# Performance work log

Hardware: AMD Instinct MI355X
Metric: run time of the kernel (lower is better)

The kernel has to match this reference:

```python
import jax, jax.numpy as jnp
import numpy as np

TWO_PI = 2.0 * np.pi
SIGMA = 25.0  # marginal_prob_std sigma


def marginal_prob_std(t):
    # std(t) = sqrt((sigma^{2t} - 1) / (2 ln sigma)) for VE-SDE
    return jnp.sqrt((SIGMA ** (2.0 * t) - 1.0) / (2.0 * np.log(SIGMA)))


def edge_conv(x, src, dst, W1, b1, W2, b2, num_nodes):
    # PyG EdgeConv: msg = mlp(cat([x_i, x_j - x_i])), x_i = x[dst], x_j = x[src];
    # scatter-max over dst. First linear split so concat is never materialized:
    # cat([x_i, x_j - x_i]) @ W1 = x_i @ (Wa - Wb) + x_j @ Wb
    d = x.shape[-1]
    Wa, Wb = W1[:d], W1[d:]
    h_center = x @ (Wa - Wb)        # [N, H]
    h_nbr = x @ Wb                  # [N, H]
    e = jax.nn.relu(h_center[dst] + h_nbr[src] + b1)  # [E, H]
    e = e @ W2 + b2                 # [E, out]
    return jax.ops.segment_max(e, dst, num_segments=num_nodes)


def setup_inputs() -> dict:
    N, E, B, H, EM = 50000, 500000, 1024, 128, 64
    CLS, SD, GD, WD = 10, 4, 2, 2
    key = jax.random.key(0)
    ks = jax.random.split(key, 32)

    def lin(k, fi, fo):
        return jax.random.normal(k, (fi, fo), jnp.float32) / np.sqrt(fi)

    inp = {
        "t": jax.random.uniform(ks[0], (N, 1), jnp.float32, 1e-3, 1.0),
        "obj_x": jax.random.normal(ks[1], (N, SD), jnp.float32),
        "obj_geo": jax.random.normal(ks[2], (N, GD), jnp.float32),
        "wall": jax.random.normal(ks[3], (B, WD), jnp.float32),
        "category": jax.random.randint(ks[4], (N,), 0, CLS),
        "batch_idx": jnp.sort(jax.random.randint(ks[5], (N,), 0, B)),
        "src": jax.random.randint(ks[6], (E,), 0, N),
        "dst": jnp.tile(jnp.arange(N), E // N),  # every node receives edges
        "embed_W": jax.random.normal(ks[7], (CLS, EM), jnp.float32),
        "gfp_W": jax.random.normal(ks[8], (EM // 2,), jnp.float32) * 30.0,
        "sW": lin(ks[9], EM, EM), "sb": jnp.zeros((EM,), jnp.float32),
        "w1": lin(ks[10], WD, EM), "wb1": jnp.zeros((EM,), jnp.float32),
        "w2": lin(ks[11], EM, EM), "wb2": jnp.zeros((EM,), jnp.float32),
        "i1": lin(ks[12], SD + GD, H), "ib1": jnp.zeros((H,), jnp.float32),
        "i2": lin(ks[13], H, H), "ib2": jnp.zeros((H,), jnp.float32),
        "m1W1": lin(ks[14], 2 * (H + 3 * EM), H), "m1b1": jnp.zeros((H,), jnp.float32),
        "m1W2": lin(ks[15], H, H), "m1b2": jnp.zeros((H,), jnp.float32),
        "m2W1": lin(ks[16], 2 * (H + 3 * EM), H), "m2b1": jnp.zeros((H,), jnp.float32),
        "m2W2": lin(ks[17], H, SD), "m2b2": jnp.zeros((SD,), jnp.float32),
    }
    return inp


def reference(t, obj_x, obj_geo, wall, category, batch_idx, src, dst,
              embed_W, gfp_W, sW, sb, w1, wb1, w2, wb2,
              i1, ib1, i2, ib2, m1W1, m1b1, m1W2, m1b2,
              m2W1, m2b1, m2W2, m2b2):
    N = obj_x.shape[0]
    # conditioning features
    class_feat = jax.nn.relu(embed_W[category])                       # [N, EM]
    tv = t[:, 0]                                                      # [N]
    x_proj = tv[:, None] * gfp_W[None, :] * TWO_PI                    # [N, EM/2]
    gfp = jnp.concatenate([jnp.sin(x_proj), jnp.cos(x_proj)], axis=-1)
    sigma_feat = jax.nn.relu(gfp @ sW + sb)                           # [N, EM]
    wall_h = jax.nn.relu(jax.nn.relu(wall @ w1 + wb1) @ w2 + wb2)     # [B, EM]
    wall_feat = wall_h[batch_idx]                                     # [N, EM]
    cond = jnp.concatenate([class_feat, sigma_feat, wall_feat], axis=-1)

    # init encoder
    xin = jnp.concatenate([obj_x, obj_geo], axis=-1)                  # [N, 6]
    init = jax.nn.relu(jax.nn.relu(xin @ i1 + ib1) @ i2 + ib2)        # [N, H]

    # main backbone: two EdgeConvs with conditioning concat
    x = jnp.concatenate([init, cond], axis=-1)                        # [N, H+3EM]
    x = jax.nn.relu(edge_conv(x, src, dst, m1W1, m1b1, m1W2, m1b2, N))
    x = jnp.concatenate([x, cond], axis=-1)                           # [N, H+3EM]
    x = edge_conv(x, src, dst, m2W1, m2b1, m2W2, m2b2, N)             # [N, 4]

    return x / (marginal_prob_std(t) + 1e-7)
```

## Files before the change

kernel.cpp:

```cpp
#include <hip/hip_runtime.h>
#include <hip/hip_bf16.h>
#include <math.h>

#define NTHREADS 256
#define TWO_PI_F 6.28318530717958647692f
#define LOG_SIGMA 3.2188758248682006f

typedef unsigned short u16;
typedef unsigned int u32;
typedef short bf16x8 __attribute__((ext_vector_type(8)));
typedef float f32x4 __attribute__((ext_vector_type(4)));

#define MFMA(a, b, c) __builtin_amdgcn_mfma_f32_16x16x32_bf16((a), (b), (c), 0, 0, 0)

__device__ __forceinline__ u16 f2b(float f) {
  __hip_bfloat16 h = __float2bfloat16(f);
  return __builtin_bit_cast(u16, h);
}
__device__ __forceinline__ u32 pk2(float lo, float hi) {
  return (u32)f2b(lo) | ((u32)f2b(hi) << 16);
}
__device__ __forceinline__ float blo(u32 u) { return __uint_as_float(u << 16); }
__device__ __forceinline__ float bhi(u32 u) { return __uint_as_float(u & 0xffff0000u); }

__global__ __launch_bounds__(256) void prep_wall_kernel(
    const float* __restrict__ m1W2, const float* __restrict__ m1W1,
    const float* __restrict__ m2W1, const float* __restrict__ sW,
    const float* __restrict__ i1, const float* __restrict__ i2,
    const float* __restrict__ wall, const float* __restrict__ w1,
    const float* __restrict__ wb1, const float* __restrict__ w2,
    const float* __restrict__ wb2,
    u16* __restrict__ m1W2t, u16* __restrict__ Wc1t, u16* __restrict__ Wc2t,
    u16* __restrict__ sWt, u16* __restrict__ i1t, u16* __restrict__ i2t,
    float* __restrict__ wall_h, int B) {
  if (blockIdx.x >= 800) {
    __shared__ float h1[4][64];
    int g = threadIdx.x >> 6, f = threadIdx.x & 63;
    int b = (blockIdx.x - 800) * 4 + g;
    if (b < B) {
      float v = wall[b * 2 + 0] * w1[f] + wall[b * 2 + 1] * w1[64 + f] + wb1[f];
      h1[g][f] = fmaxf(v, 0.f);
    }
    __syncthreads();
    if (b < B) {
      float acc = wb2[f];
      for (int k = 0; k < 64; ++k) acc = fmaf(h1[g][k], w2[k * 64 + f], acc);
      wall_h[b * 64 + f] = fmaxf(acc, 0.f);
    }
    return;
  }
  int idx = blockIdx.x * 256 + threadIdx.x;
  if (idx < 16384) {
    int n = idx >> 7, k = idx & 127;
    m1W2t[idx] = f2b(m1W2[k * 128 + n]);
  } else if (idx < 98304) {
    int j = idx - 16384;
    int n = j / 320, k = j - n * 320;
    float v = (n < 128) ? (m1W1[k * 128 + n] - m1W1[(320 + k) * 128 + n])
                        : m1W1[(320 + k) * 128 + (n - 128)];
    Wc1t[j] = f2b(v);
  } else if (idx < 180224) {
    int j = idx - 98304;
    int n = j / 320, k = j - n * 320;
    float v = (n < 128) ? (m2W1[k * 128 + n] - m2W1[(320 + k) * 128 + n])
                        : m2W1[(320 + k) * 128 + (n - 128)];
    Wc2t[j] = f2b(v);
  } else if (idx < 184320) {
    int j = idx - 180224;
    int n = j >> 6, k = j & 63;
    sWt[j] = f2b(sW[k * 64 + n]);
  } else if (idx < 188416) {
    int j = idx - 184320;
    int n = j >> 5, k = j & 31;
    i1t[j] = (k < 6) ? f2b(i1[k * 128 + n]) : (u16)0;
  } else if (idx < 204800) {
    int j = idx - 188416;
    int n = j >> 7, k = j & 127;
    i2t[j] = f2b(i2[k * 128 + n]);
  }
}

__global__ __launch_bounds__(256) void node_kernel(
    const float* __restrict__ t, const float* __restrict__ obj_x,
    const float* __restrict__ obj_geo,
    const int* __restrict__ category, const int* __restrict__ batch_idx,
    const float* __restrict__ embed_W, const float* __restrict__ gfp_W,
    const u16* __restrict__ sWt, const float* __restrict__ sb,
    const u16* __restrict__ i1t, const float* __restrict__ ib1,
    const u16* __restrict__ i2t, const float* __restrict__ ib2,
    const u16* __restrict__ Wc1t, const float* __restrict__ m1b1,
    const float* __restrict__ wall_h,
    float* __restrict__ hc1, u16* __restrict__ hn1,
    u16* __restrict__ cond_bf, int N) {
  __shared__ u16 xb[64 * 328];
  __shared__ u16 ab[64 * 136];
  __shared__ float t_s[64];
  __shared__ int cat_s[64];
  __shared__ int bid_s[64];

  const int tid = threadIdx.x;
  const int base = blockIdx.x * 64;
  const int wave = tid >> 6, lane = tid & 63;
  const int ln16 = lane & 15, q8 = lane >> 4;

  bf16x8 bs0 = *(const bf16x8*)(sWt + (size_t)((wave * 16 + ln16) * 64) + q8 * 8);
  bf16x8 bs1 = *(const bf16x8*)(sWt + (size_t)((wave * 16 + ln16) * 64) + 32 + q8 * 8);
  bf16x8 bh[2];
#pragma unroll
  for (int nt = 0; nt < 2; ++nt)
    bh[nt] = *(const bf16x8*)(i1t + (size_t)((wave * 32 + nt * 16 + ln16) * 32) + q8 * 8);

  if (tid < 64) {
    int node = min(base + tid, N - 1);
    t_s[tid] = t[node];
    cat_s[tid] = category[node];
    bid_s[tid] = batch_idx[node];
  }
  __syncthreads();

  for (int idx = tid; idx < 64 * 32; idx += NTHREADS) {
    int row = idx >> 5, k = idx & 31;
    float xp = t_s[row] * gfp_W[k] * TWO_PI_F;
    float s, c;
    sincosf(xp, &s, &c);
    ab[row * 136 + k] = f2b(s);
    ab[row * 136 + 32 + k] = f2b(c);
  }
  for (int idx = tid; idx < 64 * 64; idx += NTHREADS) {
    int row = idx >> 6, f = idx & 63;
    xb[row * 328 + 128 + f] = f2b(fmaxf(embed_W[cat_s[row] * 64 + f], 0.f));
    xb[row * 328 + 256 + f] = f2b(wall_h[bid_s[row] * 64 + f]);
  }
  __syncthreads();

  f32x4 cs[4];
#pragma unroll
  for (int mt = 0; mt < 4; ++mt) cs[mt] = (f32x4)0.f;
#pragma unroll
  for (int mt = 0; mt < 4; ++mt) {
    bf16x8 a0 = *(const bf16x8*)&ab[(mt * 16 + ln16) * 136 + q8 * 8];
    cs[mt] = MFMA(a0, bs0, cs[mt]);
  }
#pragma unroll
  for (int mt = 0; mt < 4; ++mt) {
    bf16x8 a1 = *(const bf16x8*)&ab[(mt * 16 + ln16) * 136 + 32 + q8 * 8];
    cs[mt] = MFMA(a1, bs1, cs[mt]);
  }
  __syncthreads();

  {
    int col = wave * 16 + ln16;
    float bias = sb[col];
#pragma unroll
    for (int mt = 0; mt < 4; ++mt)
#pragma unroll
      for (int r = 0; r < 4; ++r)
        xb[(mt * 16 + q8 * 4 + r) * 328 + 192 + col] = f2b(fmaxf(cs[mt][r] + bias, 0.f));
  }
  for (int idx = tid; idx < 64 * 32; idx += NTHREADS) {
    int row = idx >> 5, k = idx & 31;
    int node = min(base + row, N - 1);
    float v = (k < 4) ? obj_x[node * 4 + k] : ((k < 6) ? obj_geo[node * 2 + (k - 4)] : 0.f);
    ab[row * 136 + k] = f2b(v);
  }
  __syncthreads();

  for (int idx = tid; idx < 64 * 24; idx += NTHREADS) {
    int row = idx / 24, q = idx - row * 24;
    int node = base + row;
    if (node < N)
      *(uint4*)&cond_bf[(size_t)node * 192 + q * 8] = *(uint4*)&xb[row * 328 + 128 + q * 8];
  }

  f32x4 ch[2][4];
#pragma unroll
  for (int nt = 0; nt < 2; ++nt)
#pragma unroll
    for (int mt = 0; mt < 4; ++mt) ch[nt][mt] = (f32x4)0.f;
#pragma unroll
  for (int mt = 0; mt < 4; ++mt) {
    bf16x8 a = *(const bf16x8*)&ab[(mt * 16 + ln16) * 136 + q8 * 8];
#pragma unroll
    for (int nt = 0; nt < 2; ++nt) ch[nt][mt] = MFMA(a, bh[nt], ch[nt][mt]);
  }
  bf16x8 bcur2[2], bnext2[2];
#pragma unroll
  for (int nt = 0; nt < 2; ++nt)
    bcur2[nt] = *(const bf16x8*)(i2t + (size_t)((wave * 32 + nt * 16 + ln16) * 128) + q8 * 8);
  __syncthreads();
#pragma unroll
  for (int nt = 0; nt < 2; ++nt) {
    int col = wave * 32 + nt * 16 + ln16;
    float bias = ib1[col];
#pragma unroll
    for (int mt = 0; mt < 4; ++mt)
#pragma unroll
      for (int r = 0; r < 4; ++r)
        ab[(mt * 16 + q8 * 4 + r) * 136 + col] = f2b(fmaxf(ch[nt][mt][r] + bias, 0.f));
  }
  __syncthreads();

  f32x4 ci[2][4];
#pragma unroll
  for (int nt = 0; nt < 2; ++nt)
#pragma unroll
    for (int mt = 0; mt < 4; ++mt) ci[nt][mt] = (f32x4)0.f;
  for (int kt = 0; kt < 4; ++kt) {
    if (kt < 3) {
#pragma unroll
      for (int nt = 0; nt < 2; ++nt)
        bnext2[nt] = *(const bf16x8*)(i2t + (size_t)((wave * 32 + nt * 16 + ln16) * 128) +
                                      (kt + 1) * 32 + q8 * 8);
    }
#pragma unroll
    for (int mt = 0; mt < 4; ++mt) {
      bf16x8 a = *(const bf16x8*)&ab[(mt * 16 + ln16) * 136 + kt * 32 + q8 * 8];
#pragma unroll
      for (int nt = 0; nt < 2; ++nt) ci[nt][mt] = MFMA(a, bcur2[nt], ci[nt][mt]);
    }
#pragma unroll
    for (int nt = 0; nt < 2; ++nt) bcur2[nt] = bnext2[nt];
  }
#pragma unroll
  for (int nt = 0; nt < 2; ++nt) {
    int col = wave * 32 + nt * 16 + ln16;
    float bias = ib2[col];
#pragma unroll
    for (int mt = 0; mt < 4; ++mt)
#pragma unroll
      for (int r = 0; r < 4; ++r)
        xb[(mt * 16 + q8 * 4 + r) * 328 + col] = f2b(fmaxf(ci[nt][mt][r] + bias, 0.f));
  }
  __syncthreads();

  f32x4 c2[4][4];
#pragma unroll
  for (int nt = 0; nt < 4; ++nt)
#pragma unroll
    for (int mt = 0; mt < 4; ++mt) c2[nt][mt] = (f32x4)0.f;
  bf16x8 bcur[4], bnext[4];
#pragma unroll
  for (int nt = 0; nt < 4; ++nt)
    bcur[nt] = *(const bf16x8*)(Wc1t + (size_t)((wave * 64 + nt * 16 + ln16) * 320) + q8 * 8);
  for (int kt = 0; kt < 10; ++kt) {
    if (kt < 9) {
#pragma unroll
      for (int nt = 0; nt < 4; ++nt)
        bnext[nt] = *(const bf16x8*)(Wc1t + (size_t)((wave * 64 + nt * 16 + ln16) * 320) +
                                     (kt + 1) * 32 + q8 * 8);
    }
#pragma unroll
    for (int mt = 0; mt < 4; ++mt) {
      bf16x8 a = *(const bf16x8*)&xb[(mt * 16 + ln16) * 328 + kt * 32 + q8 * 8];
#pragma unroll
      for (int nt = 0; nt < 4; ++nt) c2[nt][mt] = MFMA(a, bcur[nt], c2[nt][mt]);
    }
#pragma unroll
    for (int nt = 0; nt < 4; ++nt) bcur[nt] = bnext[nt];
  }
#pragma unroll
  for (int nt = 0; nt < 4; ++nt) {
    int col = wave * 64 + nt * 16 + ln16;
#pragma unroll
    for (int mt = 0; mt < 4; ++mt)
#pragma unroll
      for (int r = 0; r < 4; ++r) {
        int node = base + mt * 16 + q8 * 4 + r;
        if (node < N) {
          if (col < 128)
            hc1[(size_t)node * 128 + col] = c2[nt][mt][r] + m1b1[col];
          else
            hn1[(size_t)node * 128 + (col - 128)] = f2b(c2[nt][mt][r]);
        }
      }
  }
}

__device__ __forceinline__ void pack_edge(u16* __restrict__ dst, const float* __restrict__ hcr,
                                          uint4 g0, uint4 g1, int ln, int kq) {
  float a[16];
  a[0] = blo(g0.x); a[1] = bhi(g0.x); a[2] = blo(g0.y); a[3] = bhi(g0.y);
  a[4] = blo(g0.z); a[5] = bhi(g0.z); a[6] = blo(g0.w); a[7] = bhi(g0.w);
  a[8] = blo(g1.x); a[9] = bhi(g1.x); a[10] = blo(g1.y); a[11] = bhi(g1.y);
  a[12] = blo(g1.z); a[13] = bhi(g1.z); a[14] = blo(g1.w); a[15] = bhi(g1.w);
#pragma unroll
  for (int i = 0; i < 16; ++i) a[i] = fmaxf(hcr[i] + a[i], 0.f);
  uint4 o0, o1;
  o0.x = pk2(a[0], a[1]); o0.y = pk2(a[2], a[3]); o0.z = pk2(a[4], a[5]); o0.w = pk2(a[6], a[7]);
  o1.x = pk2(a[8], a[9]); o1.y = pk2(a[10], a[11]); o1.z = pk2(a[12], a[13]); o1.w = pk2(a[14], a[15]);
  *(uint4*)&dst[ln * 136 + kq * 16] = o0;
  *(uint4*)&dst[ln * 136 + kq * 16 + 8] = o1;
}

__global__ __launch_bounds__(256) void edge1_kernel(
    const float* __restrict__ hc1, const u16* __restrict__ hn1,
    const u16* __restrict__ cond_bf, const int* __restrict__ src,
    const u16* __restrict__ m1W2t, const float* __restrict__ m1b2,
    const u16* __restrict__ Wc2t, const float* __restrict__ m2b1,
    float* __restrict__ hc2, u16* __restrict__ hn2, int N) {
  __shared__ u16 a_lds[2][32 * 136];
  __shared__ u16 x2_lds[32 * 328];
  __shared__ int sid[320];

  const int tid = threadIdx.x;
  const int base = blockIdx.x * 32;
  const int wave = tid >> 6, lane = tid & 63;
  const int ln16 = lane & 15, q8 = lane >> 4;

  for (int idx = tid; idx < 320; idx += NTHREADS) {
    int e = idx >> 5, n = idx & 31;
    int node = min(base + n, N - 1);
    sid[idx] = src[node + e * N];
  }
  for (int idx = tid; idx < 768; idx += NTHREADS) {
    int n = idx / 24, q = idx - n * 24;
    int node = min(base + n, N - 1);
    *(uint4*)&x2_lds[n * 328 + 128 + q * 8] = *(const uint4*)&cond_bf[(size_t)node * 192 + q * 8];
  }
  const int ln = tid >> 3, kq = tid & 7;
  const int lnode = min(base + ln, N - 1);
  float hcr[16];
#pragma unroll
  for (int q = 0; q < 4; ++q) {
    float4 v = *(const float4*)&hc1[(size_t)lnode * 128 + kq * 16 + q * 4];
    hcr[q * 4 + 0] = v.x; hcr[q * 4 + 1] = v.y; hcr[q * 4 + 2] = v.z; hcr[q * 4 + 3] = v.w;
  }
  bf16x8 bfrag[2][4];
#pragma unroll
  for (int nt = 0; nt < 2; ++nt)
#pragma unroll
    for (int kt = 0; kt < 4; ++kt)
      bfrag[nt][kt] = *(const bf16x8*)(m1W2t + (size_t)((2 * wave + nt) * 16 + ln16) * 128 +
                                       kt * 32 + q8 * 8);

  f32x4 ymax[2][2];
#pragma unroll
  for (int mt = 0; mt < 2; ++mt)
#pragma unroll
    for (int nt = 0; nt < 2; ++nt)
#pragma unroll
      for (int r = 0; r < 4; ++r) ymax[mt][nt][r] = -3.0e38f;

  __syncthreads();

  {
    int s0 = sid[ln];
    uint4 g0 = *(const uint4*)&hn1[(size_t)s0 * 128 + kq * 16];
    uint4 g1 = *(const uint4*)&hn1[(size_t)s0 * 128 + kq * 16 + 8];
    pack_edge(&a_lds[0][0], hcr, g0, g1, ln, kq);
  }
  uint4 gA0, gA1, gB0, gB1;
  {
    int s1 = sid[32 + ln];
    gA0 = *(const uint4*)&hn1[(size_t)s1 * 128 + kq * 16];
    gA1 = *(const uint4*)&hn1[(size_t)s1 * 128 + kq * 16 + 8];
    int s2 = sid[64 + ln];
    gB0 = *(const uint4*)&hn1[(size_t)s2 * 128 + kq * 16];
    gB1 = *(const uint4*)&hn1[(size_t)s2 * 128 + kq * 16 + 8];
  }
  asm volatile("s_waitcnt lgkmcnt(0)" ::: "memory");
  __builtin_amdgcn_s_barrier();

#pragma unroll 2
  for (int e = 0; e < 10; ++e) {
    const u16* abuf = &a_lds[e & 1][0];
    f32x4 c[2][2];
#pragma unroll
    for (int mt = 0; mt < 2; ++mt)
#pragma unroll
      for (int nt = 0; nt < 2; ++nt) c[mt][nt] = (f32x4)0.f;
#pragma unroll
    for (int kt = 0; kt < 4; ++kt) {
      bf16x8 a0 = *(const bf16x8*)&abuf[ln16 * 136 + kt * 32 + q8 * 8];
      bf16x8 a1 = *(const bf16x8*)&abuf[(16 + ln16) * 136 + kt * 32 + q8 * 8];
#pragma unroll
      for (int nt = 0; nt < 2; ++nt) {
        c[0][nt] = MFMA(a0, bfrag[nt][kt], c[0][nt]);
        c[1][nt] = MFMA(a1, bfrag[nt][kt], c[1][nt]);
      }
    }
#pragma unroll
    for (int mt = 0; mt < 2; ++mt)
#pragma unroll
      for (int nt = 0; nt < 2; ++nt)
#pragma unroll
        for (int r = 0; r < 4; ++r) ymax[mt][nt][r] = fmaxf(ymax[mt][nt][r], c[mt][nt][r]);

    if (e < 9) {
      if ((e & 1) == 0) {
        pack_edge(&a_lds[1][0], hcr, gA0, gA1, ln, kq);
        if (e + 3 < 10) {
          int s = sid[(e + 3) * 32 + ln];
          gA0 = *(const uint4*)&hn1[(size_t)s * 128 + kq * 16];
          gA1 = *(const uint4*)&hn1[(size_t)s * 128 + kq * 16 + 8];
        }
      } else {
        pack_edge(&a_lds[0][0], hcr, gB0, gB1, ln, kq);
        if (e + 3 < 10) {
          int s = sid[(e + 3) * 32 + ln];
          gB0 = *(const uint4*)&hn1[(size_t)s * 128 + kq * 16];
          gB1 = *(const uint4*)&hn1[(size_t)s * 128 + kq * 16 + 8];
        }
      }
      asm volatile("s_waitcnt lgkmcnt(0)" ::: "memory");
      __builtin_amdgcn_s_barrier();
    }
  }

#pragma unroll
  for (int mt = 0; mt < 2; ++mt)
#pragma unroll
    for (int nt = 0; nt < 2; ++nt) {
      int col = (2 * wave + nt) * 16 + ln16;
      float bias = m1b2[col];
#pragma unroll
      for (int r = 0; r < 4; ++r) {
        int row = mt * 16 + q8 * 4 + r;
        x2_lds[row * 328 + col] = f2b(fmaxf(ymax[mt][nt][r] + bias, 0.f));
      }
    }
  __syncthreads();

  f32x4 c2[2][4];
#pragma unroll
  for (int mt = 0; mt < 2; ++mt)
#pragma unroll
    for (int nt = 0; nt < 4; ++nt) c2[mt][nt] = (f32x4)0.f;
  bf16x8 bcur[4], bnext[4];
#pragma unroll
  for (int nt = 0; nt < 4; ++nt)
    bcur[nt] = *(const bf16x8*)(Wc2t + (size_t)((wave * 4 + nt) * 16 + ln16) * 320 + q8 * 8);
  for (int kt = 0; kt < 10; ++kt) {
    if (kt < 9) {
#pragma unroll
      for (int nt = 0; nt < 4; ++nt)
        bnext[nt] = *(const bf16x8*)(Wc2t + (size_t)((wave * 4 + nt) * 16 + ln16) * 320 +
                                     (kt + 1) * 32 + q8 * 8);
    }
    bf16x8 a0 = *(const bf16x8*)&x2_lds[ln16 * 328 + kt * 32 + q8 * 8];
    bf16x8 a1 = *(const bf16x8*)&x2_lds[(16 + ln16) * 328 + kt * 32 + q8 * 8];
#pragma unroll
    for (int nt = 0; nt < 4; ++nt) {
      c2[0][nt] = MFMA(a0, bcur[nt], c2[0][nt]);
      c2[1][nt] = MFMA(a1, bcur[nt], c2[1][nt]);
    }
#pragma unroll
    for (int nt = 0; nt < 4; ++nt) bcur[nt] = bnext[nt];
  }
#pragma unroll
  for (int mt = 0; mt < 2; ++mt)
#pragma unroll
    for (int nt = 0; nt < 4; ++nt) {
      int col = (wave * 4 + nt) * 16 + ln16;
#pragma unroll
      for (int r = 0; r < 4; ++r) {
        int row = mt * 16 + q8 * 4 + r;
        int node = base + row;
        if (node < N) {
          if (wave < 2)
            hc2[(size_t)node * 128 + col] = c2[mt][nt][r] + m2b1[col];
          else
            hn2[(size_t)node * 128 + (col - 128)] = f2b(c2[mt][nt][r]);
        }
      }
    }
}

__global__ __launch_bounds__(256) void edge2_kernel(
    const float* __restrict__ hc2, const u16* __restrict__ hn2,
    const int* __restrict__ src, const float* __restrict__ t,
    const float* __restrict__ m2W2, const float* __restrict__ m2b2,
    float* __restrict__ out, int N) {
  const int tid = threadIdx.x;
  const int base = blockIdx.x * 32;
  const int ln = tid >> 3, kq = tid & 7;
  const int node = min(base + ln, N - 1);

  int s[10];
#pragma unroll
  for (int e = 0; e < 10; ++e) s[e] = src[node + e * N];

  float acc[10][4];
#pragma unroll
  for (int e = 0; e < 10; ++e)
#pragma unroll
    for (int j = 0; j < 4; ++j) acc[e][j] = 0.f;

#pragma unroll
  for (int p = 0; p < 2; ++p) {
    const int d0 = p * 64 + kq * 8;
    float hcr[8];
    {
      float4 v0 = *(const float4*)&hc2[(size_t)node * 128 + d0];
      float4 v1 = *(const float4*)&hc2[(size_t)node * 128 + d0 + 4];
      hcr[0] = v0.x; hcr[1] = v0.y; hcr[2] = v0.z; hcr[3] = v0.w;
      hcr[4] = v1.x; hcr[5] = v1.y; hcr[6] = v1.z; hcr[7] = v1.w;
    }
    float w[8][4];
#pragma unroll
    for (int i = 0; i < 8; ++i) {
      float4 v = *(const float4*)&m2W2[(d0 + i) * 4];
      w[i][0] = v.x; w[i][1] = v.y; w[i][2] = v.z; w[i][3] = v.w;
    }
    uint4 gA = *(const uint4*)&hn2[(size_t)s[0] * 128 + d0];
    uint4 gB = *(const uint4*)&hn2[(size_t)s[1] * 128 + d0];
#pragma unroll
    for (int e = 0; e < 10; ++e) {
      uint4 h = (e & 1) ? gB : gA;
      if (e + 2 < 10) {
        uint4 gn = *(const uint4*)&hn2[(size_t)s[e + 2] * 128 + d0];
        if (e & 1) gB = gn; else gA = gn;
      }
      float a[8];
      a[0] = blo(h.x); a[1] = bhi(h.x); a[2] = blo(h.y); a[3] = bhi(h.y);
      a[4] = blo(h.z); a[5] = bhi(h.z); a[6] = blo(h.w); a[7] = bhi(h.w);
#pragma unroll
      for (int i = 0; i < 8; ++i) {
        float av = fmaxf(hcr[i] + a[i], 0.f);
#pragma unroll
        for (int j = 0; j < 4; ++j) acc[e][j] = fmaf(av, w[i][j], acc[e][j]);
      }
      __builtin_amdgcn_sched_barrier(0);
    }
  }

  float ymax[4] = {-3.0e38f, -3.0e38f, -3.0e38f, -3.0e38f};
#pragma unroll
  for (int e = 0; e < 10; ++e) {
    float t0 = acc[e][0], t1 = acc[e][1], t2 = acc[e][2], t3 = acc[e][3];
#pragma unroll
    for (int mask = 1; mask <= 4; mask <<= 1) {
      t0 += __shfl_xor(t0, mask);
      t1 += __shfl_xor(t1, mask);
      t2 += __shfl_xor(t2, mask);
      t3 += __shfl_xor(t3, mask);
    }
    ymax[0] = fmaxf(ymax[0], t0);
    ymax[1] = fmaxf(ymax[1], t1);
    ymax[2] = fmaxf(ymax[2], t2);
    ymax[3] = fmaxf(ymax[3], t3);
  }
  if (kq < 4 && base + ln < N) {
    float tv = t[node];
    float mps = sqrtf((expf(2.f * tv * LOG_SIGMA) - 1.f) * (1.f / (2.f * LOG_SIGMA)));
    out[(size_t)node * 4 + kq] = (ymax[kq] + m2b2[kq]) / (mps + 1e-7f);
  }
}

extern "C" void kernel_launch(void* const* d_in, const int* in_sizes, int n_in,
                              void* d_out, int out_size, void* d_ws, size_t ws_size,
                              hipStream_t stream) {
  const float* t = (const float*)d_in[0];
  const float* obj_x = (const float*)d_in[1];
  const float* obj_geo = (const float*)d_in[2];
  const float* wall = (const float*)d_in[3];
  const int* category = (const int*)d_in[4];
  const int* batch_idx = (const int*)d_in[5];
  const int* src = (const int*)d_in[6];
  const float* embed_W = (const float*)d_in[8];
  const float* gfp_W = (const float*)d_in[9];
  const float* sW = (const float*)d_in[10];
  const float* sb = (const float*)d_in[11];
  const float* w1 = (const float*)d_in[12];
  const float* wb1 = (const float*)d_in[13];
  const float* w2 = (const float*)d_in[14];
  const float* wb2 = (const float*)d_in[15];
  const float* i1 = (const float*)d_in[16];
  const float* ib1 = (const float*)d_in[17];
  const float* i2 = (const float*)d_in[18];
  const float* ib2 = (const float*)d_in[19];
  const float* m1W1 = (const float*)d_in[20];
  const float* m1b1 = (const float*)d_in[21];
  const float* m1W2 = (const float*)d_in[22];
  const float* m1b2 = (const float*)d_in[23];
  const float* m2W1 = (const float*)d_in[24];
  const float* m2b1 = (const float*)d_in[25];
  const float* m2W2 = (const float*)d_in[26];
  const float* m2b2 = (const float*)d_in[27];
  float* out = (float*)d_out;

  const int N = in_sizes[0];
  const int B = in_sizes[3] / 2;

  char* w = (char*)d_ws;
  float* wall_h = (float*)w; w += (size_t)B * 64 * 4;
  u16* cond_bf = (u16*)w;   w += (size_t)N * 192 * 2;
  float* hc1 = (float*)w;   w += (size_t)N * 128 * 4;
  u16* hn1 = (u16*)w;       w += (size_t)N * 128 * 2;
  float* hc2 = (float*)w;   w += (size_t)N * 128 * 4;
  u16* hn2 = (u16*)w;       w += (size_t)N * 128 * 2;
  u16* m1W2t = (u16*)w;     w += (size_t)128 * 128 * 2;
  u16* Wc1t = (u16*)w;      w += (size_t)256 * 320 * 2;
  u16* Wc2t = (u16*)w;      w += (size_t)256 * 320 * 2;
  u16* sWt = (u16*)w;       w += (size_t)64 * 64 * 2;
  u16* i1t = (u16*)w;       w += (size_t)128 * 32 * 2;
  u16* i2t = (u16*)w;       w += (size_t)128 * 128 * 2;

  int wall_blocks = (B + 3) / 4;
  prep_wall_kernel<<<dim3(800 + wall_blocks), dim3(256), 0, stream>>>(
      m1W2, m1W1, m2W1, sW, i1, i2, wall, w1, wb1, w2, wb2,
      m1W2t, Wc1t, Wc2t, sWt, i1t, i2t, wall_h, B);
  node_kernel<<<dim3((N + 63) / 64), dim3(NTHREADS), 0, stream>>>(
      t, obj_x, obj_geo, category, batch_idx, embed_W, gfp_W, sWt, sb,
      i1t, ib1, i2t, ib2, Wc1t, m1b1, wall_h, hc1, hn1, cond_bf, N);
  edge1_kernel<<<dim3((N + 31) / 32), dim3(NTHREADS), 0, stream>>>(
      hc1, hn1, cond_bf, src, m1W2t, m1b2, Wc2t, m2b1, hc2, hn2, N);
  edge2_kernel<<<dim3((N + 31) / 32), dim3(NTHREADS), 0, stream>>>(
      hc2, hn2, src, t, m2W2, m2b2, out, N);
}
```

Measured before the change: 270.0 us.

## Split edge1 K dimension into halves with per-edge accumulators and finer pipeline

Restructures the edge-message loop in edge1_kernel to gather and pack only half of each neighbor's 128-wide hidden row per step. It runs 20 half-K steps and keeps five per-edge MFMA accumulators, folding them into the running max after each group of five edges. This halves the LDS staging buffer and the per-step gather size, aiming at lower LDS use and a finer-grained gather/MFMA overlap. In exchange it doubles the number of barriers and adds 20 f32x4 accumulator registers, which may reduce occupancy.

```diff
diff --git a/kernel.cpp b/kernel.cpp
--- a/kernel.cpp
+++ b/kernel.cpp
@@ -276,20 +276,16 @@
   }
 }
 
-__device__ __forceinline__ void pack_edge(u16* __restrict__ dst, const float* __restrict__ hcr,
-                                          uint4 g0, uint4 g1, int ln, int kq) {
-  float a[16];
-  a[0] = blo(g0.x); a[1] = bhi(g0.x); a[2] = blo(g0.y); a[3] = bhi(g0.y);
-  a[4] = blo(g0.z); a[5] = bhi(g0.z); a[6] = blo(g0.w); a[7] = bhi(g0.w);
-  a[8] = blo(g1.x); a[9] = bhi(g1.x); a[10] = blo(g1.y); a[11] = bhi(g1.y);
-  a[12] = blo(g1.z); a[13] = bhi(g1.z); a[14] = blo(g1.w); a[15] = bhi(g1.w);
-#pragma unroll
-  for (int i = 0; i < 16; ++i) a[i] = fmaxf(hcr[i] + a[i], 0.f);
-  uint4 o0, o1;
-  o0.x = pk2(a[0], a[1]); o0.y = pk2(a[2], a[3]); o0.z = pk2(a[4], a[5]); o0.w = pk2(a[6], a[7]);
-  o1.x = pk2(a[8], a[9]); o1.y = pk2(a[10], a[11]); o1.z = pk2(a[12], a[13]); o1.w = pk2(a[14], a[15]);
-  *(uint4*)&dst[ln * 136 + kq * 16] = o0;
-  *(uint4*)&dst[ln * 136 + kq * 16 + 8] = o1;
+__device__ __forceinline__ void pack_half(u16* __restrict__ dst, const float* __restrict__ hcr8,
+                                          uint4 h, int ln, int kq) {
+  float a[8];
+  a[0] = blo(h.x); a[1] = bhi(h.x); a[2] = blo(h.y); a[3] = bhi(h.y);
+  a[4] = blo(h.z); a[5] = bhi(h.z); a[6] = blo(h.w); a[7] = bhi(h.w);
+#pragma unroll
+  for (int i = 0; i < 8; ++i) a[i] = fmaxf(hcr8[i] + a[i], 0.f);
+  uint4 o;
+  o.x = pk2(a[0], a[1]); o.y = pk2(a[2], a[3]); o.z = pk2(a[4], a[5]); o.w = pk2(a[6], a[7]);
+  *(uint4*)&dst[ln * 72 + kq * 8] = o;
 }
 
 __global__ __launch_bounds__(256) void edge1_kernel(
@@ -298,7 +294,7 @@
     const u16* __restrict__ m1W2t, const float* __restrict__ m1b2,
     const u16* __restrict__ Wc2t, const float* __restrict__ m2b1,
     float* __restrict__ hc2, u16* __restrict__ hn2, int N) {
-  __shared__ u16 a_lds[2][32 * 136];
+  __shared__ u16 a_lds[2][32 * 72];
   __shared__ u16 x2_lds[32 * 328];
   __shared__ int sid[320];
 
@@ -321,9 +317,11 @@
   const int lnode = min(base + ln, N - 1);
   float hcr[16];
 #pragma unroll
-  for (int q = 0; q < 4; ++q) {
-    float4 v = *(const float4*)&hc1[(size_t)lnode * 128 + kq * 16 + q * 4];
-    hcr[q * 4 + 0] = v.x; hcr[q * 4 + 1] = v.y; hcr[q * 4 + 2] = v.z; hcr[q * 4 + 3] = v.w;
+  for (int p = 0; p < 2; ++p) {
+    float4 v0 = *(const float4*)&hc1[(size_t)lnode * 128 + p * 64 + kq * 8];
+    float4 v1 = *(const float4*)&hc1[(size_t)lnode * 128 + p * 64 + kq * 8 + 4];
+    hcr[p * 8 + 0] = v0.x; hcr[p * 8 + 1] = v0.y; hcr[p * 8 + 2] = v0.z; hcr[p * 8 + 3] = v0.w;
+    hcr[p * 8 + 4] = v1.x; hcr[p * 8 + 5] = v1.y; hcr[p * 8 + 6] = v1.z; hcr[p * 8 + 7] = v1.w;
   }
   bf16x8 bfrag[2][4];
 #pragma unroll
@@ -341,70 +339,75 @@
 #pragma unroll
       for (int r = 0; r < 4; ++r) ymax[mt][nt][r] = -3.0e38f;
 
+  f32x4 acc[5][2][2];
+#pragma unroll
+  for (int e = 0; e < 5; ++e)
+#pragma unroll
+    for (int mt = 0; mt < 2; ++mt)
+#pragma unroll
+      for (int nt = 0; nt < 2; ++nt) acc[e][mt][nt] = (f32x4)0.f;
+
   __syncthreads();
 
   {
     int s0 = sid[ln];
-    uint4 g0 = *(const uint4*)&hn1[(size_t)s0 * 128 + kq * 16];
-    uint4 g1 = *(const uint4*)&hn1[(size_t)s0 * 128 + kq * 16 + 8];
-    pack_edge(&a_lds[0][0], hcr, g0, g1, ln, kq);
-  }
-  uint4 gA0, gA1, gB0, gB1;
+    uint4 h = *(const uint4*)&hn1[(size_t)s0 * 128 + kq * 8];
+    pack_half(&a_lds[0][0], &hcr[0], h, ln, kq);
+  }
+  uint4 sA, sB;
   {
-    int s1 = sid[32 + ln];
-    gA0 = *(const uint4*)&hn1[(size_t)s1 * 128 + kq * 16];
-    gA1 = *(const uint4*)&hn1[(size_t)s1 * 128 + kq * 16 + 8];
-    int s2 = sid[64 + ln];
-    gB0 = *(const uint4*)&hn1[(size_t)s2 * 128 + kq * 16];
-    gB1 = *(const uint4*)&hn1[(size_t)s2 * 128 + kq * 16 + 8];
+    int s1 = sid[1 * 32 + ln];
+    sA = *(const uint4*)&hn1[(size_t)s1 * 128 + kq * 8];
+    int s2 = sid[2 * 32 + ln];
+    sB = *(const uint4*)&hn1[(size_t)s2 * 128 + kq * 8];
   }
   asm volatile("s_waitcnt lgkmcnt(0)" ::: "memory");
   __builtin_amdgcn_s_barrier();
 
-#pragma unroll 2
-  for (int e = 0; e < 10; ++e) {
-    const u16* abuf = &a_lds[e & 1][0];
-    f32x4 c[2][2];
-#pragma unroll
-    for (int mt = 0; mt < 2; ++mt)
-#pragma unroll
-      for (int nt = 0; nt < 2; ++nt) c[mt][nt] = (f32x4)0.f;
-#pragma unroll
-    for (int kt = 0; kt < 4; ++kt) {
-      bf16x8 a0 = *(const bf16x8*)&abuf[ln16 * 136 + kt * 32 + q8 * 8];
-      bf16x8 a1 = *(const bf16x8*)&abuf[(16 + ln16) * 136 + kt * 32 + q8 * 8];
+#pragma unroll
+  for (int it = 0; it < 20; ++it) {
+    const int p = (it % 10) / 5, e = it % 5;
+    const u16* abuf = &a_lds[it & 1][0];
+#pragma unroll
+    for (int kt = 0; kt < 2; ++kt) {
+      bf16x8 a0 = *(const bf16x8*)&abuf[ln16 * 72 + kt * 32 + q8 * 8];
+      bf16x8 a1 = *(const bf16x8*)&abuf[(16 + ln16) * 72 + kt * 32 + q8 * 8];
 #pragma unroll
       for (int nt = 0; nt < 2; ++nt) {
-        c[0][nt] = MFMA(a0, bfrag[nt][kt], c[0][nt]);
-        c[1][nt] = MFMA(a1, bfrag[nt][kt], c[1][nt]);
+        acc[e][0][nt] = MFMA(a0, bfrag[nt][p * 2 + kt], acc[e][0][nt]);
+        acc[e][1][nt] = MFMA(a1, bfrag[nt][p * 2 + kt], acc[e][1][nt]);
       }
     }
-#pragma unroll
-    for (int mt = 0; mt < 2; ++mt)
-#pragma unroll
-      for (int nt = 0; nt < 2; ++nt)
-#pragma unroll
-        for (int r = 0; r < 4; ++r) ymax[mt][nt][r] = fmaxf(ymax[mt][nt][r], c[mt][nt][r]);
-
-    if (e < 9) {
-      if ((e & 1) == 0) {
-        pack_edge(&a_lds[1][0], hcr, gA0, gA1, ln, kq);
-        if (e + 3 < 10) {
-          int s = sid[(e + 3) * 32 + ln];
-          gA0 = *(const uint4*)&hn1[(size_t)s * 128 + kq * 16];
-          gA1 = *(const uint4*)&hn1[(size_t)s * 128 + kq * 16 + 8];
-        }
-      } else {
-        pack_edge(&a_lds[0][0], hcr, gB0, gB1, ln, kq);
-        if (e + 3 < 10) {
-          int s = sid[(e + 3) * 32 + ln];
-          gB0 = *(const uint4*)&hn1[(size_t)s * 128 + kq * 16];
-          gB1 = *(const uint4*)&hn1[(size_t)s * 128 + kq * 16 + 8];
-        }
+    if (it == 9 || it == 19) {
+#pragma unroll
+      for (int ee = 0; ee < 5; ++ee)
+#pragma unroll
+        for (int mt = 0; mt < 2; ++mt)
+#pragma unroll
+          for (int nt = 0; nt < 2; ++nt) {
+#pragma unroll
+            for (int r = 0; r < 4; ++r)
+              ymax[mt][nt][r] = fmaxf(ymax[mt][nt][r], acc[ee][mt][nt][r]);
+            acc[ee][mt][nt] = (f32x4)0.f;
+          }
+    }
+    if (it < 19) {
+      const int itn = it + 1;
+      const int pn = (itn % 10) / 5, edn = (itn / 10) * 5 + itn % 5;
+      (void)edn;
+      uint4 h = (itn & 1) ? sA : sB;
+      pack_half(&a_lds[itn & 1][0], &hcr[pn * 8], h, ln, kq);
+      if (it + 3 <= 19) {
+        const int itf = it + 3;
+        const int pf = (itf % 10) / 5, edf = (itf / 10) * 5 + itf % 5;
+        int s = sid[edf * 32 + ln];
+        uint4 gn = *(const uint4*)&hn1[(size_t)s * 128 + pf * 64 + kq * 8];
+        if (itf & 1) sA = gn; else sB = gn;
       }
       asm volatile("s_waitcnt lgkmcnt(0)" ::: "memory");
       __builtin_amdgcn_s_barrier();
     }
+    __builtin_amdgcn_sched_barrier(0);
   }
 
 #pragma unroll
```

Result: slower. 282.0 us (+4.5%).
